# Performance work log

Measured on AMD Instinct MI355X. Metric: run time of the kernel, lower is better.

## Reference

```python
import jax, jax.numpy as jnp
import numpy as np

NUM_NODES = 100000
NUM_EDGES = 1600000
NUM_GRAPHS = 64
IN_DIM = 128
HID = 128
OUT_DIM = 256
NUM_LAYERS = 5
BN_EPS = 1e-5


def _bn(t, gamma, beta):
    # BatchNorm1d forward with batch statistics (biased variance), as in train mode
    m = jnp.mean(t, axis=0)
    v = jnp.var(t, axis=0)
    return gamma * (t - m) * jax.lax.rsqrt(v + BN_EPS) + beta


def setup_inputs() -> dict:
    key = jax.random.key(0)
    ks = jax.random.split(key, 16)
    x = jax.random.normal(ks[0], (NUM_NODES, IN_DIM), dtype=jnp.float32)
    edge_index = jax.random.randint(ks[1], (2, NUM_EDGES), 0, NUM_NODES, dtype=jnp.int64)
    batch = jnp.sort(jax.random.randint(ks[2], (NUM_NODES,), 0, NUM_GRAPHS, dtype=jnp.int64))
    s1 = 1.0 / np.sqrt(IN_DIM)
    s2 = 1.0 / np.sqrt(HID)
    # stacked per-layer GIN MLP params: Linear(HID,HID) -> BN -> ReLU -> Linear(HID,HID)
    w1 = jax.random.normal(ks[3], (NUM_LAYERS, HID, HID), dtype=jnp.float32) * s1
    b1 = jnp.zeros((NUM_LAYERS, HID), dtype=jnp.float32)
    gamma1 = jnp.ones((NUM_LAYERS, HID), dtype=jnp.float32)
    beta1 = jnp.zeros((NUM_LAYERS, HID), dtype=jnp.float32)
    w2 = jax.random.normal(ks[4], (NUM_LAYERS, HID, HID), dtype=jnp.float32) * s2
    b2 = jnp.zeros((NUM_LAYERS, HID), dtype=jnp.float32)
    # outer per-layer BatchNorm after each GINConv
    gamma_bn = jnp.ones((NUM_LAYERS, HID), dtype=jnp.float32)
    beta_bn = jnp.zeros((NUM_LAYERS, HID), dtype=jnp.float32)
    # output projection Linear(HID, OUT_DIM)
    wp = jax.random.normal(ks[5], (HID, OUT_DIM), dtype=jnp.float32) * s2
    bp = jnp.zeros((OUT_DIM,), dtype=jnp.float32)
    return {"x": x, "edge_index": edge_index, "batch": batch,
            "w1": w1, "b1": b1, "gamma1": gamma1, "beta1": beta1,
            "w2": w2, "b2": b2, "gamma_bn": gamma_bn, "beta_bn": beta_bn,
            "wp": wp, "bp": bp}


def reference(x, edge_index, batch, w1, b1, gamma1, beta1, w2, b2, gamma_bn, beta_bn, wp, bp):
    src, dst = edge_index[0], edge_index[1]
    h = x
    for i in range(NUM_LAYERS):
        # GINConv, eps=0: mlp((1+eps)*h + sum_{j in N(i)} h_j)
        agg = jax.ops.segment_sum(h[src], dst, num_segments=NUM_NODES)
        z = h + agg
        t = _bn(z @ w1[i] + b1[i], gamma1[i], beta1[i])
        t = jax.nn.relu(t)
        t = t @ w2[i] + b2[i]
        # outer BatchNorm + ReLU (dropout p handled as identity in eval)
        t = jax.nn.relu(_bn(t, gamma_bn[i], beta_bn[i]))
        h = h + t  # residual (dims always match)
    node_emb = h
    # global mean pool per graph
    sums = jax.ops.segment_sum(h, batch, num_segments=NUM_GRAPHS)
    counts = jax.ops.segment_sum(jnp.ones((NUM_NODES,), dtype=h.dtype), batch, num_segments=NUM_GRAPHS)
    pooled = sums / jnp.maximum(counts, 1.0)[:, None]
    graph_emb = pooled @ wp + bp
    return graph_emb, node_emb
```

## Files before the change

kernel.cpp:

```cpp
#include <hip/hip_runtime.h>

#define NNODES 100000
#define NEDGES 1600000
#define NGRAPHS 64
#define HID 128
#define OUTD 256
#define NLAYERS 5
#define BN_EPS 1e-5f
#define NBUCK 196
#define BUCKCAP 9216
#define FILL_BLOCKS 391
#define NREP 8

typedef __attribute__((ext_vector_type(8))) short short8;
typedef __attribute__((ext_vector_type(4))) float f32x4;

__device__ inline unsigned short f2b(float f) {
    union { float f; unsigned int u; } a; a.f = f;
    unsigned int u = a.u;
    return (unsigned short)((u + 0x7FFF + ((u >> 16) & 1)) >> 16);
}
__device__ inline float b2f(unsigned short b) {
    union { unsigned int u; float f; } a; a.u = ((unsigned int)b) << 16;
    return a.f;
}

__global__ void k_init(const float* __restrict__ x, float* __restrict__ h,
                       ushort* __restrict__ hb) {
    int i = blockIdx.x * 256 + threadIdx.x;
    float4 v = ((const float4*)x)[i];
    ((float4*)h)[i] = v;
    ushort4 o;
    o.x = f2b(v.x); o.y = f2b(v.y); o.z = f2b(v.z); o.w = f2b(v.w);
    ((ushort4*)hb)[i] = o;
}

__global__ void k_bcur0(int* __restrict__ bcur) {
    int t = threadIdx.x;
    if (t < NBUCK) bcur[t] = t * BUCKCAP;
}

__global__ __launch_bounds__(256) void k_fill1(
    const int* __restrict__ srcv, const int* __restrict__ dstv,
    int* __restrict__ bcur, unsigned int* __restrict__ packed) {
    __shared__ int hist[NBUCK];
    __shared__ int base[NBUCK];
    int tid = threadIdx.x;
    int e0 = blockIdx.x * 4096;
    for (int i = tid; i < NBUCK; i += 256) hist[i] = 0;
    __syncthreads();
#pragma unroll
    for (int i = 0; i < 16; i++) {
        int e = e0 + i * 256 + tid;
        if (e < NEDGES) atomicAdd(&hist[dstv[e] >> 9], 1);
    }
    __syncthreads();
    for (int i = tid; i < NBUCK; i += 256) {
        int c = hist[i];
        base[i] = c ? atomicAdd(&bcur[i], c) : 0;
        hist[i] = 0;
    }
    __syncthreads();
#pragma unroll
    for (int i = 0; i < 16; i++) {
        int e = e0 + i * 256 + tid;
        if (e < NEDGES) {
            int d = dstv[e];
            int b = d >> 9;
            int r = atomicAdd(&hist[b], 1);
            packed[base[b] + r] = ((unsigned int)srcv[e] << 9) | (unsigned int)(d & 511);
        }
    }
}

__global__ __launch_bounds__(256) void k_fill2(
    const unsigned int* __restrict__ packed, const int* __restrict__ bcur,
    int2* __restrict__ off2, int* __restrict__ adj) {
    __shared__ int deg[512];
    __shared__ int cur[512];
    int tid = threadIdx.x;
    int b = blockIdx.x;
    int base = b * BUCKCAP;
    int cnt = bcur[b] - base;
    deg[tid] = 0; deg[tid + 256] = 0;
    __syncthreads();
    for (int i = tid; i < cnt; i += 256)
        atomicAdd(&deg[packed[base + i] & 511], 1);
    __syncthreads();
    cur[tid] = deg[tid]; cur[tid + 256] = deg[tid + 256];
    __syncthreads();
    for (int o = 1; o < 512; o <<= 1) {
        int u0 = (tid >= o) ? cur[tid - o] : 0;
        int u1 = (tid + 256 >= o) ? cur[tid + 256 - o] : 0;
        __syncthreads();
        cur[tid] += u0; cur[tid + 256] += u1;
        __syncthreads();
    }
    int nbase = b * 512;
#pragma unroll
    for (int i = 0; i < 2; i++) {
        int t = tid + i * 256;
        int st = base + cur[t] - deg[t];
        int n = nbase + t;
        if (n < NNODES) off2[n] = make_int2(st, st + deg[t]);
    }
    __syncthreads();
#pragma unroll
    for (int i = 0; i < 2; i++) {
        int t = tid + i * 256;
        cur[t] = base + cur[t] - deg[t];
    }
    __syncthreads();
    for (int i = tid; i < cnt; i += 256) {
        unsigned int p = packed[base + i];
        int r = atomicAdd(&cur[p & 511], 1);
        adj[r] = (int)(p >> 9);
    }
}

__global__ void k_wt(const float* __restrict__ w1, const float* __restrict__ w2,
                     unsigned short* __restrict__ WT) {
    int t = blockIdx.x * 256 + threadIdx.x;
    int mat = t >> 14;
    int rem = t & 16383;
    int k = rem >> 7, n = rem & 127;
    const float* src = (mat < 5) ? &w1[(size_t)mat * 16384] : &w2[(size_t)(mat - 5) * 16384];
    WT[(size_t)mat * 16384 + n * 128 + k] = f2b(src[k * 128 + n]);
}

__global__ void k_agg(const ushort* __restrict__ hb, const int2* __restrict__ off2,
                      const int* __restrict__ adj, ushort* __restrict__ zb) {
    int tid = threadIdx.x;
    int node = blockIdx.x * 8 + (tid >> 5);
    int d4 = tid & 31;
    const ushort4* hb4 = (const ushort4*)hb;
    ushort4 sv = hb4[(size_t)node * 32 + d4];
    float4 v = make_float4(b2f(sv.x), b2f(sv.y), b2f(sv.z), b2f(sv.w));
    int2 oo = off2[node];
    int e = oo.x, e1 = oo.y;
    for (; e + 8 <= e1; e += 8) {
        int s[8]; ushort4 u[8];
#pragma unroll
        for (int j = 0; j < 8; j++) s[j] = adj[e + j];
#pragma unroll
        for (int j = 0; j < 8; j++) u[j] = hb4[(size_t)s[j] * 32 + d4];
#pragma unroll
        for (int j = 0; j < 8; j++) {
            v.x += b2f(u[j].x); v.y += b2f(u[j].y);
            v.z += b2f(u[j].z); v.w += b2f(u[j].w);
        }
    }
    for (; e + 4 <= e1; e += 4) {
        int s0 = adj[e], s1 = adj[e + 1], s2 = adj[e + 2], s3 = adj[e + 3];
        ushort4 u0 = hb4[(size_t)s0 * 32 + d4];
        ushort4 u1 = hb4[(size_t)s1 * 32 + d4];
        ushort4 u2 = hb4[(size_t)s2 * 32 + d4];
        ushort4 u3 = hb4[(size_t)s3 * 32 + d4];
        v.x += (b2f(u0.x) + b2f(u1.x)) + (b2f(u2.x) + b2f(u3.x));
        v.y += (b2f(u0.y) + b2f(u1.y)) + (b2f(u2.y) + b2f(u3.y));
        v.z += (b2f(u0.z) + b2f(u1.z)) + (b2f(u2.z) + b2f(u3.z));
        v.w += (b2f(u0.w) + b2f(u1.w)) + (b2f(u2.w) + b2f(u3.w));
    }
    for (; e < e1; e++) {
        int s = adj[e];
        ushort4 u = hb4[(size_t)s * 32 + d4];
        v.x += b2f(u.x); v.y += b2f(u.y); v.z += b2f(u.z); v.w += b2f(u.w);
    }
    ushort4 o;
    o.x = f2b(v.x); o.y = f2b(v.y); o.z = f2b(v.z); o.w = f2b(v.w);
    ((ushort4*)zb)[(size_t)node * 32 + d4] = o;
}

__global__ __launch_bounds__(256) void k_gemm1(
    const ushort* __restrict__ A, const unsigned short* __restrict__ WT,
    const float* __restrict__ bias, ushort* __restrict__ C,
    float* __restrict__ stats) {
    __shared__ float lstat[256];
    int tid = threadIdx.x;
    int wave = tid >> 6;
    int lane = tid & 63;
    int q = lane >> 4;
    int l16 = lane & 15;
    int rowbase = blockIdx.x * 128 + wave * 32;

    f32x4 acc[2][8];
#pragma unroll
    for (int rt = 0; rt < 2; rt++)
#pragma unroll
        for (int nt = 0; nt < 8; nt++) acc[rt][nt] = (f32x4){0.f, 0.f, 0.f, 0.f};

    for (int kc = 0; kc < 4; kc++) {
        int k0 = kc * 32 + q * 8;
        short8 bf[8];
#pragma unroll
        for (int nt = 0; nt < 8; nt++)
            bf[nt] = *(const short8*)&WT[(size_t)(nt * 16 + l16) * 128 + k0];
#pragma unroll
        for (int rt = 0; rt < 2; rt++) {
            int row = rowbase + rt * 16 + l16;
            if (row >= NNODES) row = NNODES - 1;
            short8 av = *(const short8*)&A[(size_t)row * 128 + k0];
#pragma unroll
            for (int nt = 0; nt < 8; nt++)
                acc[rt][nt] = __builtin_amdgcn_mfma_f32_16x16x32_bf16(
                    av, bf[nt], acc[rt][nt], 0, 0, 0);
        }
    }

    lstat[tid] = 0.f;
    __syncthreads();
#pragma unroll
    for (int nt = 0; nt < 8; nt++) {
        float b = bias[nt * 16 + l16];
        float csum = 0.f, csq = 0.f;
#pragma unroll
        for (int rt = 0; rt < 2; rt++) {
            int rb = rowbase + rt * 16 + q * 4;
#pragma unroll
            for (int r = 0; r < 4; r++) {
                int row = rb + r;
                if (row < NNODES) {
                    float v = acc[rt][nt][r] + b;
                    C[(size_t)row * 128 + nt * 16 + l16] = f2b(v);
                    csum += v; csq += v * v;
                }
            }
        }
        csum += __shfl_xor(csum, 16, 64); csq += __shfl_xor(csq, 16, 64);
        csum += __shfl_xor(csum, 32, 64); csq += __shfl_xor(csq, 32, 64);
        if (q == 0) {
            atomicAdd(&lstat[nt * 16 + l16], csum);
            atomicAdd(&lstat[128 + nt * 16 + l16], csq);
        }
    }
    __syncthreads();
    atomicAdd(&stats[((blockIdx.x & (NREP - 1)) << 8) + tid], lstat[tid]);
}

__global__ __launch_bounds__(256) void k_gemm2(
    const ushort* __restrict__ A, const unsigned short* __restrict__ WT,
    const float* __restrict__ bias, ushort* __restrict__ C,
    const float* __restrict__ statsIn, const float* __restrict__ gamma,
    const float* __restrict__ beta, float* __restrict__ stats) {
    __shared__ float lstat[256];
    __shared__ float s_sc[128], s_sh[128];
    int tid = threadIdx.x;
    if (tid < 128) {
        float s = 0.f, qq = 0.f;
#pragma unroll
        for (int r = 0; r < NREP; r++) {
            s  += statsIn[r * 256 + tid];
            qq += statsIn[r * 256 + 128 + tid];
        }
        float m = s * (1.f / NNODES);
        float var = qq * (1.f / NNODES) - m * m;
        float sc = gamma[tid] * rsqrtf(var + BN_EPS);
        s_sc[tid] = sc;
        s_sh[tid] = beta[tid] - m * sc;
    }
    __syncthreads();

    int wave = tid >> 6;
    int lane = tid & 63;
    int q = lane >> 4;
    int l16 = lane & 15;
    int rowbase = blockIdx.x * 128 + wave * 32;

    f32x4 acc[2][8];
#pragma unroll
    for (int rt = 0; rt < 2; rt++)
#pragma unroll
        for (int nt = 0; nt < 8; nt++) acc[rt][nt] = (f32x4){0.f, 0.f, 0.f, 0.f};

    for (int kc = 0; kc < 4; kc++) {
        int k0 = kc * 32 + q * 8;
        short8 bf[8];
#pragma unroll
        for (int nt = 0; nt < 8; nt++)
            bf[nt] = *(const short8*)&WT[(size_t)(nt * 16 + l16) * 128 + k0];

        float4 s0 = *(const float4*)&s_sc[k0];
        float4 s1 = *(const float4*)&s_sc[k0 + 4];
        float4 t0 = *(const float4*)&s_sh[k0];
        float4 t1 = *(const float4*)&s_sh[k0 + 4];
        float scl[8] = {s0.x, s0.y, s0.z, s0.w, s1.x, s1.y, s1.z, s1.w};
        float shf[8] = {t0.x, t0.y, t0.z, t0.w, t1.x, t1.y, t1.z, t1.w};
#pragma unroll
        for (int rt = 0; rt < 2; rt++) {
            int row = rowbase + rt * 16 + l16;
            if (row >= NNODES) row = NNODES - 1;
            union { short8 s; unsigned short u[8]; } in, cv;
            in.s = *(const short8*)&A[(size_t)row * 128 + k0];
#pragma unroll
            for (int j = 0; j < 8; j++) {
                float f = fmaxf(b2f(in.u[j]) * scl[j] + shf[j], 0.f);
                cv.u[j] = f2b(f);
            }
#pragma unroll
            for (int nt = 0; nt < 8; nt++)
                acc[rt][nt] = __builtin_amdgcn_mfma_f32_16x16x32_bf16(
                    cv.s, bf[nt], acc[rt][nt], 0, 0, 0);
        }
    }

    lstat[tid] = 0.f;
    __syncthreads();
#pragma unroll
    for (int nt = 0; nt < 8; nt++) {
        float b = bias[nt * 16 + l16];
        float csum = 0.f, csq = 0.f;
#pragma unroll
        for (int rt = 0; rt < 2; rt++) {
            int rb = rowbase + rt * 16 + q * 4;
#pragma unroll
            for (int r = 0; r < 4; r++) {
                int row = rb + r;
                if (row < NNODES) {
                    float v = acc[rt][nt][r] + b;
                    C[(size_t)row * 128 + nt * 16 + l16] = f2b(v);
                    csum += v; csq += v * v;
                }
            }
        }
        csum += __shfl_xor(csum, 16, 64); csq += __shfl_xor(csq, 16, 64);
        csum += __shfl_xor(csum, 32, 64); csq += __shfl_xor(csq, 32, 64);
        if (q == 0) {
            atomicAdd(&lstat[nt * 16 + l16], csum);
            atomicAdd(&lstat[128 + nt * 16 + l16], csq);
        }
    }
    __syncthreads();
    atomicAdd(&stats[((blockIdx.x & (NREP - 1)) << 8) + tid], lstat[tid]);
}

__global__ void k_resid(float* __restrict__ h, ushort* __restrict__ hb,
                        const ushort* __restrict__ t2b,
                        const float* __restrict__ statsIn,
                        const float* __restrict__ gamma, const float* __restrict__ beta) {
    __shared__ float s_sc[128], s_sh[128];
    int tid = threadIdx.x;
    if (tid < 128) {
        float s = 0.f, qq = 0.f;
#pragma unroll
        for (int r = 0; r < NREP; r++) {
            s  += statsIn[r * 256 + tid];
            qq += statsIn[r * 256 + 128 + tid];
        }
        float m = s * (1.f / NNODES);
        float var = qq * (1.f / NNODES) - m * m;
        float sc = gamma[tid] * rsqrtf(var + BN_EPS);
        s_sc[tid] = sc;
        s_sh[tid] = beta[tid] - m * sc;
    }
    __syncthreads();
    int i = blockIdx.x * 256 + tid;
    int c4 = (i & 31) * 4;
    float4 sc = *(const float4*)&s_sc[c4];
    float4 sh = *(const float4*)&s_sh[c4];
    ushort4 t = ((const ushort4*)t2b)[i];
    float4 hv = ((float4*)h)[i];
    hv.x += fmaxf(b2f(t.x) * sc.x + sh.x, 0.f);
    hv.y += fmaxf(b2f(t.y) * sc.y + sh.y, 0.f);
    hv.z += fmaxf(b2f(t.z) * sc.z + sh.z, 0.f);
    hv.w += fmaxf(b2f(t.w) * sc.w + sh.w, 0.f);
    ((float4*)h)[i] = hv;
    ushort4 o;
    o.x = f2b(hv.x); o.y = f2b(hv.y); o.z = f2b(hv.z); o.w = f2b(hv.w);
    ((ushort4*)hb)[i] = o;
}

__global__ void k_counts(const int* __restrict__ batch, float* __restrict__ cnt) {
    int g = threadIdx.x;
    if (g >= NGRAPHS) return;
    auto lb = [&](int key) {
        int lo = 0, hi = NNODES;
        while (lo < hi) {
            int mid = (lo + hi) >> 1;
            if (batch[mid] < key) lo = mid + 1; else hi = mid;
        }
        return lo;
    };
    cnt[g] = (float)(lb(g + 1) - lb(g));
}

__global__ void k_pool(const float* __restrict__ h, const int* __restrict__ batch,
                       float* __restrict__ pooled) {
    __shared__ float4 red[256];
    int t = threadIdx.x;
    int d4 = t & 31, sub = t >> 5;
    int n0 = blockIdx.x * 128;
    if (n0 >= NNODES) return;
    int n1 = n0 + 128; if (n1 > NNODES) n1 = NNODES;
    int glo = batch[n0], ghi = batch[n1 - 1];
    for (int g = glo; g <= ghi; g++) {
        float4 acc = make_float4(0.f, 0.f, 0.f, 0.f);
        for (int r = n0 + sub; r < n1; r += 8) {
            if (batch[r] == g) {
                float4 v = ((const float4*)h)[(size_t)r * 32 + d4];
                acc.x += v.x; acc.y += v.y; acc.z += v.z; acc.w += v.w;
            }
        }
        red[t] = acc;
        __syncthreads();
        if (sub < 4) {
            float4 o = red[t + 128];
            red[t].x += o.x; red[t].y += o.y; red[t].z += o.z; red[t].w += o.w;
        }
        __syncthreads();
        if (sub < 2) {
            float4 o = red[t + 64];
            red[t].x += o.x; red[t].y += o.y; red[t].z += o.z; red[t].w += o.w;
        }
        __syncthreads();
        if (sub == 0) {
            float4 o = red[t + 32];
            float4 a = red[t];
            a.x += o.x; a.y += o.y; a.z += o.z; a.w += o.w;
            atomicAdd(&pooled[g * 128 + d4 * 4 + 0], a.x);
            atomicAdd(&pooled[g * 128 + d4 * 4 + 1], a.y);
            atomicAdd(&pooled[g * 128 + d4 * 4 + 2], a.z);
            atomicAdd(&pooled[g * 128 + d4 * 4 + 3], a.w);
        }
        __syncthreads();
    }
}

__global__ void k_proj(const float* __restrict__ pooled, const float* __restrict__ cnt,
                       const float* __restrict__ wp, const float* __restrict__ bp,
                       float* __restrict__ out) {
    __shared__ float prow[128];
    int g = blockIdx.x, c = threadIdx.x;
    if (c < 128) prow[c] = pooled[g * 128 + c] / fmaxf(cnt[g], 1.f);
    __syncthreads();
    float acc = bp[c];
    for (int k = 0; k < 128; k++) acc += prow[k] * wp[k * 256 + c];
    out[g * 256 + c] = acc;
}

extern "C" void kernel_launch(void* const* d_in, const int* in_sizes, int n_in,
                              void* d_out, int out_size, void* d_ws, size_t ws_size,
                              hipStream_t stream) {
    const float* x    = (const float*)d_in[0];
    const int*   eidx = (const int*)d_in[1];
    const int*   batch= (const int*)d_in[2];
    const float* w1   = (const float*)d_in[3];
    const float* b1   = (const float*)d_in[4];
    const float* g1   = (const float*)d_in[5];
    const float* be1  = (const float*)d_in[6];
    const float* w2   = (const float*)d_in[7];
    const float* b2   = (const float*)d_in[8];
    const float* gbn  = (const float*)d_in[9];
    const float* bbn  = (const float*)d_in[10];
    const float* wp   = (const float*)d_in[11];
    const float* bp   = (const float*)d_in[12];

    float* out  = (float*)d_out;
    float* gemb = out;
    float* h    = out + (size_t)NGRAPHS * OUTD;

    char* w = (char*)d_ws;
    ushort* hb   = (ushort*)w; w += (size_t)NNODES * 128 * 2;
    ushort* zb   = (ushort*)w; w += (size_t)NNODES * 128 * 2;
    ushort* tb   = (ushort*)w; w += (size_t)NNODES * 128 * 2;
    ushort* t2b  = (ushort*)w; w += (size_t)NNODES * 128 * 2;
    int2*  off2  = (int2*)w;  w += (size_t)NNODES * 8;
    int*   adj   = (int*)w;   w += (size_t)NBUCK * BUCKCAP * 4;
    unsigned short* WT = (unsigned short*)w; w += (size_t)10 * 16384 * 2;
    int*   bcur  = (int*)w;   w += 256 * 4;
    float* statsAll = (float*)w; w += (size_t)10 * NREP * 256 * 4;
    float* pooled= (float*)w; w += (size_t)NGRAPHS * HID * 4;
    float* gcnt  = (float*)w; w += NGRAPHS * 4;

    unsigned int* packed = (unsigned int*)tb;

    const int* srcv = eidx;
    const int* dstv = eidx + NEDGES;

    k_init<<<NNODES * 32 / 256, 256, 0, stream>>>(x, h, hb);

    k_wt<<<640, 256, 0, stream>>>(w1, w2, WT);

    hipMemsetAsync(statsAll, 0,
                   ((size_t)10 * NREP * 256 + NGRAPHS * HID + NGRAPHS) * 4, stream);

    k_bcur0<<<1, 256, 0, stream>>>(bcur);
    k_fill1<<<FILL_BLOCKS, 256, 0, stream>>>(srcv, dstv, bcur, packed);
    k_fill2<<<NBUCK, 256, 0, stream>>>(packed, bcur, off2, adj);

    const int GB = (NNODES + 127) / 128;
    for (int i = 0; i < NLAYERS; i++) {
        float* st1 = statsAll + (size_t)(2 * i) * NREP * 256;
        float* st2 = statsAll + (size_t)(2 * i + 1) * NREP * 256;
        k_agg<<<NNODES / 8, 256, 0, stream>>>(hb, off2, adj, zb);
        k_gemm1<<<GB, 256, 0, stream>>>(
            zb, WT + (size_t)i * 16384, b1 + i * HID, tb, st1);
        k_gemm2<<<GB, 256, 0, stream>>>(
            tb, WT + (size_t)(5 + i) * 16384, b2 + i * HID, t2b,
            st1, g1 + i * HID, be1 + i * HID, st2);
        k_resid<<<NNODES * 128 / 4 / 256, 256, 0, stream>>>(
            h, hb, t2b, st2, gbn + i * HID, bbn + i * HID);
    }

    k_counts<<<1, 64, 0, stream>>>(batch, gcnt);
    k_pool<<<(NNODES + 127) / 128, 256, 0, stream>>>(h, batch, pooled);
    k_proj<<<NGRAPHS, 256, 0, stream>>>(pooled, gcnt, wp, bp, gemb);
}
```

Baseline: 1.065 ms.

## Widen aggregation gathers to 16-byte loads and fold small setup kernels together

The aggregation kernel now has each thread handle 8 bf16 features through one short8 load per neighbor, with 16 lanes per node and 16 nodes per block, replacing 8-byte ushort4 gathers. This cuts the number of gather instructions on the dominant memory-bound step. The weight transpose is merged into the init kernel and the graph-count kernel is folded into pooling via shared-memory atomics, removing launches. The t2b buffer now aliases zb to shrink the workspace, which relies on zb being dead by the time gemm2 writes t2b.

```diff
diff --git a/kernel.cpp b/kernel.cpp
--- a/kernel.cpp
+++ b/kernel.cpp
@@ -25,14 +25,29 @@
     return a.f;
 }
 
+union U8 { short8 v; unsigned short u[8]; };
+
 __global__ void k_init(const float* __restrict__ x, float* __restrict__ h,
-                       ushort* __restrict__ hb) {
-    int i = blockIdx.x * 256 + threadIdx.x;
-    float4 v = ((const float4*)x)[i];
-    ((float4*)h)[i] = v;
-    ushort4 o;
-    o.x = f2b(v.x); o.y = f2b(v.y); o.z = f2b(v.z); o.w = f2b(v.w);
-    ((ushort4*)hb)[i] = o;
+                       ushort* __restrict__ hb,
+                       const float* __restrict__ w1, const float* __restrict__ w2,
+                       unsigned short* __restrict__ WT) {
+    int b = blockIdx.x;
+    if (b < 12500) {
+        int i = b * 256 + threadIdx.x;
+        float4 v = ((const float4*)x)[i];
+        ((float4*)h)[i] = v;
+        ushort4 o;
+        o.x = f2b(v.x); o.y = f2b(v.y); o.z = f2b(v.z); o.w = f2b(v.w);
+        ((ushort4*)hb)[i] = o;
+    } else {
+        int t = (b - 12500) * 256 + threadIdx.x;
+        int mat = t >> 14;
+        int rem = t & 16383;
+        int k = rem >> 7, n = rem & 127;
+        const float* src = (mat < 5) ? &w1[(size_t)mat * 16384]
+                                     : &w2[(size_t)(mat - 5) * 16384];
+        WT[(size_t)mat * 16384 + n * 128 + k] = f2b(src[k * 128 + n]);
+    }
 }
 
 __global__ void k_bcur0(int* __restrict__ bcur) {
@@ -118,57 +133,57 @@
     }
 }
 
-__global__ void k_wt(const float* __restrict__ w1, const float* __restrict__ w2,
-                     unsigned short* __restrict__ WT) {
-    int t = blockIdx.x * 256 + threadIdx.x;
-    int mat = t >> 14;
-    int rem = t & 16383;
-    int k = rem >> 7, n = rem & 127;
-    const float* src = (mat < 5) ? &w1[(size_t)mat * 16384] : &w2[(size_t)(mat - 5) * 16384];
-    WT[(size_t)mat * 16384 + n * 128 + k] = f2b(src[k * 128 + n]);
-}
-
-__global__ void k_agg(const ushort* __restrict__ hb, const int2* __restrict__ off2,
-                      const int* __restrict__ adj, ushort* __restrict__ zb) {
+__global__ __launch_bounds__(256) void k_agg(const ushort* __restrict__ hb,
+                                             const int2* __restrict__ off2,
+                                             const int* __restrict__ adj,
+                                             ushort* __restrict__ zb) {
     int tid = threadIdx.x;
-    int node = blockIdx.x * 8 + (tid >> 5);
-    int d4 = tid & 31;
-    const ushort4* hb4 = (const ushort4*)hb;
-    ushort4 sv = hb4[(size_t)node * 32 + d4];
-    float4 v = make_float4(b2f(sv.x), b2f(sv.y), b2f(sv.z), b2f(sv.w));
+    int node = blockIdx.x * 16 + (tid >> 4);
+    int c = tid & 15;
+    const short8* hb8 = (const short8*)hb;
+    size_t self = (size_t)node * 16 + c;
+
+    U8 sv; sv.v = hb8[self];
+    float acc[8];
+#pragma unroll
+    for (int k = 0; k < 8; k++) acc[k] = b2f(sv.u[k]);
+
     int2 oo = off2[node];
     int e = oo.x, e1 = oo.y;
     for (; e + 8 <= e1; e += 8) {
-        int s[8]; ushort4 u[8];
+        int s[8];
 #pragma unroll
         for (int j = 0; j < 8; j++) s[j] = adj[e + j];
-#pragma unroll
-        for (int j = 0; j < 8; j++) u[j] = hb4[(size_t)s[j] * 32 + d4];
-#pragma unroll
-        for (int j = 0; j < 8; j++) {
-            v.x += b2f(u[j].x); v.y += b2f(u[j].y);
-            v.z += b2f(u[j].z); v.w += b2f(u[j].w);
-        }
+        U8 u[8];
+#pragma unroll
+        for (int j = 0; j < 8; j++) u[j].v = hb8[(size_t)s[j] * 16 + c];
+#pragma unroll
+        for (int j = 0; j < 8; j++)
+#pragma unroll
+            for (int k = 0; k < 8; k++) acc[k] += b2f(u[j].u[k]);
     }
     for (; e + 4 <= e1; e += 4) {
         int s0 = adj[e], s1 = adj[e + 1], s2 = adj[e + 2], s3 = adj[e + 3];
-        ushort4 u0 = hb4[(size_t)s0 * 32 + d4];
-        ushort4 u1 = hb4[(size_t)s1 * 32 + d4];
-        ushort4 u2 = hb4[(size_t)s2 * 32 + d4];
-        ushort4 u3 = hb4[(size_t)s3 * 32 + d4];
-        v.x += (b2f(u0.x) + b2f(u1.x)) + (b2f(u2.x) + b2f(u3.x));
-        v.y += (b2f(u0.y) + b2f(u1.y)) + (b2f(u2.y) + b2f(u3.y));
-        v.z += (b2f(u0.z) + b2f(u1.z)) + (b2f(u2.z) + b2f(u3.z));
-        v.w += (b2f(u0.w) + b2f(u1.w)) + (b2f(u2.w) + b2f(u3.w));
+        U8 u0, u1, u2, u3;
+        u0.v = hb8[(size_t)s0 * 16 + c];
+        u1.v = hb8[(size_t)s1 * 16 + c];
+        u2.v = hb8[(size_t)s2 * 16 + c];
+        u3.v = hb8[(size_t)s3 * 16 + c];
+#pragma unroll
+        for (int k = 0; k < 8; k++)
+            acc[k] += (b2f(u0.u[k]) + b2f(u1.u[k])) + (b2f(u2.u[k]) + b2f(u3.u[k]));
     }
     for (; e < e1; e++) {
         int s = adj[e];
-        ushort4 u = hb4[(size_t)s * 32 + d4];
-        v.x += b2f(u.x); v.y += b2f(u.y); v.z += b2f(u.z); v.w += b2f(u.w);
-    }
-    ushort4 o;
-    o.x = f2b(v.x); o.y = f2b(v.y); o.z = f2b(v.z); o.w = f2b(v.w);
-    ((ushort4*)zb)[(size_t)node * 32 + d4] = o;
+        U8 u; u.v = hb8[(size_t)s * 16 + c];
+#pragma unroll
+        for (int k = 0; k < 8; k++) acc[k] += b2f(u.u[k]);
+    }
+
+    U8 o;
+#pragma unroll
+    for (int k = 0; k < 8; k++) o.u[k] = f2b(acc[k]);
+    ((short8*)zb)[self] = o.v;
 }
 
 __global__ __launch_bounds__(256) void k_gemm1(
@@ -369,28 +384,21 @@
     ((ushort4*)hb)[i] = o;
 }
 
-__global__ void k_counts(const int* __restrict__ batch, float* __restrict__ cnt) {
-    int g = threadIdx.x;
-    if (g >= NGRAPHS) return;
-    auto lb = [&](int key) {
-        int lo = 0, hi = NNODES;
-        while (lo < hi) {
-            int mid = (lo + hi) >> 1;
-            if (batch[mid] < key) lo = mid + 1; else hi = mid;
-        }
-        return lo;
-    };
-    cnt[g] = (float)(lb(g + 1) - lb(g));
-}
-
 __global__ void k_pool(const float* __restrict__ h, const int* __restrict__ batch,
-                       float* __restrict__ pooled) {
+                       float* __restrict__ pooled, float* __restrict__ gcnt) {
     __shared__ float4 red[256];
+    __shared__ int lcnt[NGRAPHS];
     int t = threadIdx.x;
     int d4 = t & 31, sub = t >> 5;
     int n0 = blockIdx.x * 128;
     if (n0 >= NNODES) return;
     int n1 = n0 + 128; if (n1 > NNODES) n1 = NNODES;
+    if (t < NGRAPHS) lcnt[t] = 0;
+    __syncthreads();
+    if (t < n1 - n0) atomicAdd(&lcnt[batch[n0 + t]], 1);
+    __syncthreads();
+    if (t < NGRAPHS && lcnt[t]) atomicAdd(&gcnt[t], (float)lcnt[t]);
+
     int glo = batch[n0], ghi = batch[n1 - 1];
     for (int g = glo; g <= ghi; g++) {
         float4 acc = make_float4(0.f, 0.f, 0.f, 0.f);
@@ -462,7 +470,6 @@
     ushort* hb   = (ushort*)w; w += (size_t)NNODES * 128 * 2;
     ushort* zb   = (ushort*)w; w += (size_t)NNODES * 128 * 2;
     ushort* tb   = (ushort*)w; w += (size_t)NNODES * 128 * 2;
-    ushort* t2b  = (ushort*)w; w += (size_t)NNODES * 128 * 2;
     int2*  off2  = (int2*)w;  w += (size_t)NNODES * 8;
     int*   adj   = (int*)w;   w += (size_t)NBUCK * BUCKCAP * 4;
     unsigned short* WT = (unsigned short*)w; w += (size_t)10 * 16384 * 2;
@@ -471,14 +478,13 @@
     float* pooled= (float*)w; w += (size_t)NGRAPHS * HID * 4;
     float* gcnt  = (float*)w; w += NGRAPHS * 4;
 
+    ushort* t2b = zb;
     unsigned int* packed = (unsigned int*)tb;
 
     const int* srcv = eidx;
     const int* dstv = eidx + NEDGES;
 
-    k_init<<<NNODES * 32 / 256, 256, 0, stream>>>(x, h, hb);
-
-    k_wt<<<640, 256, 0, stream>>>(w1, w2, WT);
+    k_init<<<12500 + 640, 256, 0, stream>>>(x, h, hb, w1, w2, WT);
 
     hipMemsetAsync(statsAll, 0,
                    ((size_t)10 * NREP * 256 + NGRAPHS * HID + NGRAPHS) * 4, stream);
@@ -491,7 +497,7 @@
     for (int i = 0; i < NLAYERS; i++) {
         float* st1 = statsAll + (size_t)(2 * i) * NREP * 256;
         float* st2 = statsAll + (size_t)(2 * i + 1) * NREP * 256;
-        k_agg<<<NNODES / 8, 256, 0, stream>>>(hb, off2, adj, zb);
+        k_agg<<<NNODES / 16, 256, 0, stream>>>(hb, off2, adj, zb);
         k_gemm1<<<GB, 256, 0, stream>>>(
             zb, WT + (size_t)i * 16384, b1 + i * HID, tb, st1);
         k_gemm2<<<GB, 256, 0, stream>>>(
@@ -501,7 +507,6 @@
             h, hb, t2b, st2, gbn + i * HID, bbn + i * HID);
     }
 
-    k_counts<<<1, 64, 0, stream>>>(batch, gcnt);
-    k_pool<<<(NNODES + 127) / 128, 256, 0, stream>>>(h, batch, pooled);
+    k_pool<<<(NNODES + 127) / 128, 256, 0, stream>>>(h, batch, pooled, gcnt);
     k_proj<<<NGRAPHS, 256, 0, stream>>>(pooled, gcnt, wp, bp, gemb);
 }
```

New measurement: 1.050 ms. No clear change (-1.4%).
